# Kernel optimization log

Measured on AMD Instinct MI355X. Metric: run time of the kernel, lower is better.

## Reference

```python
import jax, jax.numpy as jnp
import numpy as np

N_S, N_G, D, K = 30000, 3000, 128, 16
SIGMA = 2.5
BOX = 60.0  # Angstrom box for random coordinates


def setup_inputs() -> dict:
    key = jax.random.key(0)
    ks = jax.random.split(key, 10)
    s = 1.0 / np.sqrt(D)
    return {
        'xs': jax.random.normal(ks[0], (N_S, D), jnp.float32),
        'xg': jax.random.normal(ks[1], (N_G, D), jnp.float32),
        'pos_s': jax.random.uniform(ks[2], (N_S, 3), jnp.float32) * BOX,
        'pos_g': jax.random.uniform(ks[3], (N_G, 3), jnp.float32) * BOX,
        'W_s_pre': jax.random.normal(ks[4], (D, D), jnp.float32) * s,
        'W_g_pre': jax.random.normal(ks[5], (D, D), jnp.float32) * s,
        'W_gs': jax.random.normal(ks[6], (D, D), jnp.float32) * s,
        'W_sg': jax.random.normal(ks[7], (D, D), jnp.float32) * s,
        'W_s_post': jax.random.normal(ks[8], (2 * D, D), jnp.float32) * s,
        'W_g_post': jax.random.normal(ks[9], (2 * D, D), jnp.float32) * s,
        'k': K,
    }


def reference(xs, xg, pos_s, pos_g, W_s_pre, W_g_pre, W_gs, W_sg, W_s_post, W_g_post, k):
    n_s, d = xs.shape
    # ---- compute_bipartite_graphs: knn of each graph node over surface nodes ----
    # squared pairwise distances via gemm form: (N_G, N_S)
    d2 = ((pos_g ** 2).sum(-1)[:, None] + (pos_s ** 2).sum(-1)[None, :]
          - 2.0 * pos_g @ pos_s.T)
    neg_d2, idx = jax.lax.top_k(-d2, k)          # idx: (N_G, K) surface neighbors
    w = jnp.exp(neg_d2 / (2.0 * SIGMA ** 2))     # RBF edge weight exp(-d^2/(2*sigma^2))
    # ---- pre blocks ----
    hs = xs @ W_s_pre                             # (N_S, D)
    hg = xg @ W_g_pre                             # (N_G, D)
    # ---- bp_gs block: graph -> surface weighted edge-conv (scatter-add) ----
    msg_gs = (hg @ W_gs)[:, None, :] * w[:, :, None]          # (N_G, K, D)
    xs_out = jnp.zeros((n_s, d), hs.dtype).at[idx.reshape(-1)].add(
        msg_gs.reshape(-1, d))
    # ---- bp_sg block: surface -> graph weighted edge-conv (gather-sum) ----
    xg_out = ((hs @ W_sg)[idx] * w[:, :, None]).sum(axis=1)   # (N_G, D)
    # ---- post blocks: combine pre features with message output ----
    xs_new = jax.nn.relu(jnp.concatenate([hs, xs_out], axis=-1) @ W_s_post)
    xg_new = jax.nn.relu(jnp.concatenate([hg, xg_out], axis=-1) @ W_g_post)
    return xs_new, xg_new
```

## Files before the change

### kernel.cpp

```cpp
#include <hip/hip_runtime.h>
#include <stdint.h>

#define N_S 30000
#define N_G 3000
#define DD  128
#define KK  16
#define NE  (N_G * KK)
#define NC  16
#define CELLS (NC * NC * NC)
#define CH  3.75f
#define CAP 32

#define FILL_BLOCKS 118
#define PACK_BLOCKS 384
#define KNN_BLOCKS  750
#define NBS 469
#define NBG 47
#define NTILE (NBS + NBG)

using v8s = __attribute__((ext_vector_type(8))) short;
using v4f = __attribute__((ext_vector_type(4))) float;

__device__ __forceinline__ float bf2f(unsigned short u) {
    union { unsigned int i; float f; } v; v.i = ((unsigned int)u) << 16; return v.f;
}
__device__ __forceinline__ unsigned short f2bf(float f) {
    union { float f; unsigned int i; } v; v.f = f;
    unsigned int x = v.i;
    return (unsigned short)((x + 0x7fffu + ((x >> 16) & 1u)) >> 16);
}
__device__ __forceinline__ float ldIn(const void* p, int i, int bf) {
    return bf ? bf2f(((const unsigned short*)p)[i]) : ((const float*)p)[i];
}
__device__ __forceinline__ void stOut(void* p, int i, float v, int bf) {
    if (bf) ((unsigned short*)p)[i] = f2bf(v);
    else    ((float*)p)[i] = v;
}
__device__ __forceinline__ int cellOf(float x) {
    int c = (int)(x * (1.0f / CH));
    if (c < 0) c = 0; if (c > NC - 1) c = NC - 1;
    return c;
}

__device__ __forceinline__ int detectFlag(const void* pos_g) {
    const unsigned int* w = (const unsigned int*)pos_g;
    int votes = 0;
#pragma unroll
    for (int i = 0; i < 16; ++i) {
        const unsigned int b = (w[i] >> 8) & 0xFFu;
        votes += (b >= 0x3Eu && b <= 0x42u) ? 1 : 0;
    }
    return votes >= 8;
}

__device__ void knn_wave(int g, int bf, const void* pos_g,
                         const int* __restrict__ ccnt,
                         const float4* __restrict__ scell,
                         const float4* __restrict__ ovf, int novf,
                         int* __restrict__ idx_out, float* __restrict__ w_out)
{
    const int t = threadIdx.x & 63;

    const float gxf = ldIn(pos_g, 3 * g + 0, bf);
    const float gyf = ldIn(pos_g, 3 * g + 1, bf);
    const float gzf = ldIn(pos_g, 3 * g + 2, bf);
    const double gx = (double)gxf, gy = (double)gyf, gz = (double)gzf;
    const int cx = cellOf(gxf), cy = cellOf(gyf), cz = cellOf(gzf);

    double bk[KK]; int bi[KK];
#pragma unroll
    for (int j = 0; j < KK; ++j) { bk[j] = 1e300; bi[j] = 0x7fffffff; }

    for (int i = t; i < novf; i += 64) {
        const float4 cd = ovf[i];
        const double ddx = gx - (double)cd.x, ddy = gy - (double)cd.y, ddz = gz - (double)cd.z;
        const double d2 = ddx * ddx + ddy * ddy + ddz * ddz;
        const int sidx = __float_as_int(cd.w);
        if (d2 > bk[KK - 1] || (d2 == bk[KK - 1] && sidx > bi[KK - 1])) continue;
        double ck = d2; int ci2 = sidx;
#pragma unroll
        for (int j = 0; j < KK; ++j) {
            const bool less = (ck < bk[j]) || (ck == bk[j] && ci2 < bi[j]);
            const double nk = less ? ck : bk[j]; const int ni = less ? ci2 : bi[j];
            const double ok = less ? bk[j] : ck; const int oi = less ? bi[j] : ci2;
            bk[j] = nk; bi[j] = ni; ck = ok; ci2 = oi;
        }
    }

    bool done = false;
    for (int R = 1; R <= NC && !done; ++R) {
        const int S = 2 * R + 1;
        const int Scells = S * S * S;
        for (int cb = 0; cb < Scells; cb += 64) {
            const int ci = cb + t;
            int cnt = 0, base = 0;
            if (ci < Scells) {
                const int dz = ci % S - R;
                const int dy = (ci / S) % S - R;
                const int dx = ci / (S * S) - R;
                int ax = dx < 0 ? -dx : dx, ay = dy < 0 ? -dy : dy, az = dz < 0 ? -dz : dz;
                int cheb = ax > ay ? ax : ay; if (az > cheb) cheb = az;
                const bool want = (R == 1) ? true : (cheb == R);
                const int X = cx + dx, Y = cy + dy, Z = cz + dz;
                if (want && X >= 0 && X < NC && Y >= 0 && Y < NC && Z >= 0 && Z < NC) {
                    const int cid = (X * NC + Y) * NC + Z;
                    int c = ccnt[cid]; if (c > CAP) c = CAP;
                    cnt = c; base = cid * CAP;
                }
            }
            for (int i = 0; i < cnt; ++i) {
                const float4 cd = scell[base + i];
                const double ddx = gx - (double)cd.x;
                const double ddy = gy - (double)cd.y;
                const double ddz = gz - (double)cd.z;
                const double d2 = ddx * ddx + ddy * ddy + ddz * ddz;
                const int sidx = __float_as_int(cd.w);
                if (d2 > bk[KK - 1]) continue;
                if (d2 == bk[KK - 1] && sidx > bi[KK - 1]) continue;
                double ck = d2; int ci2 = sidx;
#pragma unroll
                for (int j = 0; j < KK; ++j) {
                    const bool less = (ck < bk[j]) || (ck == bk[j] && ci2 < bi[j]);
                    const double nk = less ? ck : bk[j]; const int ni = less ? ci2 : bi[j];
                    const double ok = less ? bk[j] : ck; const int oi = less ? bi[j] : ci2;
                    bk[j] = nk; bi[j] = ni; ck = ok; ci2 = oi;
                }
            }
        }
        double m = 1e300;
        if (cx - R > 0)      { double d = gx - (double)(cx - R) * 3.75; if (d < m) m = d; }
        if (cx + R < NC - 1) { double d = (double)(cx + R + 1) * 3.75 - gx; if (d < m) m = d; }
        if (cy - R > 0)      { double d = gy - (double)(cy - R) * 3.75; if (d < m) m = d; }
        if (cy + R < NC - 1) { double d = (double)(cy + R + 1) * 3.75 - gy; if (d < m) m = d; }
        if (cz - R > 0)      { double d = gz - (double)(cz - R) * 3.75; if (d < m) m = d; }
        if (cz + R < NC - 1) { double d = (double)(cz + R + 1) * 3.75 - gz; if (d < m) m = d; }
        if (m < 0.0) m = 0.0;
        const double m2 = m * m * (1.0 - 1e-12);
        int cntlt = 0;
#pragma unroll
        for (int j = 0; j < KK; ++j) cntlt += (bk[j] < m2) ? 1 : 0;
        for (int d = 1; d < 64; d <<= 1) cntlt += __shfl_xor(cntlt, d);
        if (cntlt >= KK) done = true;
    }

    for (int p = 0; p < KK; ++p) {
        double key = bk[0]; int sid = bi[0];
        for (int d = 1; d < 64; d <<= 1) {
            const double ok = __shfl_xor(key, d);
            const int    os = __shfl_xor(sid, d);
            if (ok < key || (ok == key && os < sid)) { key = ok; sid = os; }
        }
        if (t == 0) {
            idx_out[g * KK + p] = sid;
            w_out[g * KK + p] = expf((float)(-key) * (1.0f / 12.5f));
        }
        const bool win = (bk[0] == key) && (bi[0] == sid);
        if (win) {
#pragma unroll
            for (int j = 0; j < KK - 1; ++j) { bk[j] = bk[j + 1]; bi[j] = bi[j + 1]; }
            bk[KK - 1] = 1e300; bi[KK - 1] = 0x7fffffff;
        }
    }
}

__device__ __forceinline__ v8s loadA_bf16(const unsigned short* p) {
    return *(const v8s*)p;
}
__device__ __forceinline__ v8s loadA_f32v(const float* f) {
    const float4 a = *(const float4*)f;
    const float4 b = *(const float4*)(f + 4);
    v8s r;
    r[0] = (short)f2bf(a.x); r[1] = (short)f2bf(a.y);
    r[2] = (short)f2bf(a.z); r[3] = (short)f2bf(a.w);
    r[4] = (short)f2bf(b.x); r[5] = (short)f2bf(b.y);
    r[6] = (short)f2bf(b.z); r[7] = (short)f2bf(b.w);
    return r;
}
__device__ __forceinline__ v8s loadA_raw(const void* A, size_t off, int bf) {
    if (bf) return loadA_bf16((const unsigned short*)A + off);
    return loadA_f32v((const float*)A + off);
}

__device__ void pre_tile(int task, int bf, const void* xs, const void* xg,
                         const unsigned short* __restrict__ wpk_ps,
                         const unsigned short* __restrict__ wpk_pg,
                         unsigned short* __restrict__ hsb,
                         unsigned short* __restrict__ hgb,
                         float* __restrict__ xs_agg)
{
    const void* A; const unsigned short* wpk; unsigned short* outp; int M, m0;
    const bool is_s = (task < NBS);
    if (is_s) { A = xs; wpk = wpk_ps; outp = hsb; M = N_S; m0 = task * 64; }
    else      { A = xg; wpk = wpk_pg; outp = hgb; M = N_G; m0 = (task - NBS) * 64; }

    const int wave = threadIdx.x >> 6, lane = threadIdx.x & 63;
    const int q = lane >> 4, lm = lane & 15;
    const int mb = m0 + wave * 16;
    const int mrow = mb + lm;
    const bool valid = (mrow < M);

    v4f acc[8];
#pragma unroll
    for (int t = 0; t < 8; ++t) acc[t] = {0.f, 0.f, 0.f, 0.f};
    for (int ks = 0; ks < 4; ++ks) {
        v8s a = {0,0,0,0,0,0,0,0};
        if (valid) a = loadA_raw(A, (size_t)mrow * 128 + ks * 32 + q * 8, bf);
        const unsigned short* wb = wpk + (size_t)(ks * 4 + q) * 128 * 8;
#pragma unroll
        for (int t = 0; t < 8; ++t) {
            const v8s bfr = *(const v8s*)(wb + (t * 16 + lm) * 8);
            acc[t] = __builtin_amdgcn_mfma_f32_16x16x32_bf16(a, bfr, acc[t], 0, 0, 0);
        }
    }
#pragma unroll
    for (int t = 0; t < 8; ++t)
#pragma unroll
        for (int r = 0; r < 4; ++r) {
            const int row = mb + q * 4 + r;
            if (row < M) outp[(size_t)row * 128 + t * 16 + lm] = f2bf(acc[t][r]);
        }
    if (is_s) {
        for (int i = threadIdx.x; i < 64 * 128; i += 256) {
            const int r = m0 + (i >> 7);
            if (r < N_S) xs_agg[(size_t)r * 128 + (i & 127)] = 0.f;
        }
    }
}

__device__ void post_tile(int task, int bf,
                          const unsigned short* __restrict__ hsb,
                          const float* __restrict__ xs_agg,
                          const unsigned short* __restrict__ hgb,
                          const unsigned short* __restrict__ aggg,
                          const unsigned short* __restrict__ wpk_cs,
                          const unsigned short* __restrict__ wpk_cg,
                          void* out)
{
    const unsigned short* A1; const void* A2; int a2f32; const unsigned short* wpk;
    int M, m0, ooff;
    if (task < NBS) { A1 = hsb; A2 = xs_agg; a2f32 = 1; wpk = wpk_cs; M = N_S; m0 = task * 64; ooff = 0; }
    else { A1 = hgb; A2 = aggg; a2f32 = 0; wpk = wpk_cg; M = N_G; m0 = (task - NBS) * 64; ooff = N_S * DD; }

    const int wave = threadIdx.x >> 6, lane = threadIdx.x & 63;
    const int q = lane >> 4, lm = lane & 15;
    const int mb = m0 + wave * 16;
    const int mrow = mb + lm;
    const bool valid = (mrow < M);

    v4f acc[8];
#pragma unroll
    for (int t = 0; t < 8; ++t) acc[t] = {0.f, 0.f, 0.f, 0.f};
    for (int ks = 0; ks < 8; ++ks) {
        const int kk = ks * 32 + q * 8;
        v8s a = {0,0,0,0,0,0,0,0};
        if (valid) {
            if (kk < 128)      a = loadA_bf16(A1 + (size_t)mrow * 128 + kk);
            else if (a2f32)    a = loadA_f32v((const float*)A2 + (size_t)mrow * 128 + (kk - 128));
            else               a = loadA_bf16((const unsigned short*)A2 + (size_t)mrow * 128 + (kk - 128));
        }
        const unsigned short* wb = wpk + (size_t)(ks * 4 + q) * 128 * 8;
#pragma unroll
        for (int t = 0; t < 8; ++t) {
            const v8s bfr = *(const v8s*)(wb + (t * 16 + lm) * 8);
            acc[t] = __builtin_amdgcn_mfma_f32_16x16x32_bf16(a, bfr, acc[t], 0, 0, 0);
        }
    }
#pragma unroll
    for (int t = 0; t < 8; ++t)
#pragma unroll
        for (int r = 0; r < 4; ++r) {
            const int row = mb + q * 4 + r;
            if (row < M) {
                float v = acc[t][r];
                if (v < 0.f) v = 0.f;
                stOut(out, ooff + row * DD + t * 16 + lm, v, bf);
            }
        }
}

__global__ __launch_bounds__(256) void fill_pack_kernel(
    const void* pos_s, const void* pos_g,
    const void* Wsp, const void* Wgp, const void* Wgs, const void* Wsg,
    const void* Wspost, const void* Wgpost,
    int* __restrict__ ccnt, float4* __restrict__ scell,
    float4* __restrict__ ovf, int* __restrict__ novf,
    unsigned short* __restrict__ wpk_ps, unsigned short* __restrict__ wpk_pg,
    unsigned short* __restrict__ wpk_cs, unsigned short* __restrict__ wpk_cg)
{
    const int bf = detectFlag(pos_g);
    const int bid = blockIdx.x, tid = threadIdx.x;
    if (bid < FILL_BLOCKS) {
        const int p = bid * 256 + tid;
        if (p < N_S) {
            const float x = ldIn(pos_s, 3 * p + 0, bf);
            const float y = ldIn(pos_s, 3 * p + 1, bf);
            const float z = ldIn(pos_s, 3 * p + 2, bf);
            const int cid = (cellOf(x) * NC + cellOf(y)) * NC + cellOf(z);
            const int slot = atomicAdd(&ccnt[cid], 1);
            const float4 pt = make_float4(x, y, z, __int_as_float(p));
            if (slot < CAP) scell[cid * CAP + slot] = pt;
            else            ovf[atomicAdd(novf, 1)] = pt;
        }
        return;
    }
    __shared__ float rows[256];
    const int rt = bid - FILL_BLOCKS;
    const int half = tid >> 7, j = tid & 127;
    const int task = rt * 2 + half;
    float v; unsigned short* dst; int k;
    if (task < 128) { k = task; v = ldIn(Wsp, k * DD + j, bf); dst = wpk_ps; }
    else if (task < 256) { k = task - 128; v = ldIn(Wgp, k * DD + j, bf); dst = wpk_pg; }
    else {
        const int which_g = (task >= 512);
        const int r = which_g ? (task - 512) : (task - 256);
        const void* W1 = which_g ? Wsg : Wgs;
        const void* Wp = which_g ? Wgpost : Wspost;
        dst = which_g ? wpk_cg : wpk_cs;
        k = r;
        if (r < 128) v = ldIn(Wp, r * DD + j, bf);
        else {
            rows[half * 128 + j] = ldIn(W1, (r - 128) * DD + j, bf);
            __syncthreads();
            float acc = 0.f;
            for (int m = 0; m < DD; ++m)
                acc += rows[half * 128 + m] * ldIn(Wp, (DD + m) * DD + j, bf);
            v = acc;
        }
    }
    const int ks = k >> 5, q = (k >> 3) & 3, i = k & 7;
    dst[((ks * 4 + q) * 128 + j) * 8 + i] = f2bf(v);
}

__global__ __launch_bounds__(256) void knn_pre_kernel(
    const void* xs, const void* xg, const void* pos_g,
    const int* __restrict__ ccnt, const float4* __restrict__ scell,
    const float4* __restrict__ ovf, const int* __restrict__ novf,
    int* __restrict__ idx, float* __restrict__ w,
    const unsigned short* __restrict__ wpk_ps,
    const unsigned short* __restrict__ wpk_pg,
    unsigned short* __restrict__ hsb, unsigned short* __restrict__ hgb,
    float* __restrict__ xs_agg)
{
    const int bf = detectFlag(pos_g);
    const int bid = blockIdx.x;
    if (bid < KNN_BLOCKS) {
        const int node = bid * 4 + (threadIdx.x >> 6);
        knn_wave(node, bf, pos_g, ccnt, scell, ovf, *novf, idx, w);
    } else {
        pre_tile(bid - KNN_BLOCKS, bf, xs, xg, wpk_ps, wpk_pg, hsb, hgb, xs_agg);
    }
}

__global__ __launch_bounds__(128) void scatgath_kernel(
    const void* pos_g,
    const unsigned short* __restrict__ hsb, const unsigned short* __restrict__ hgb,
    const int* __restrict__ idx, const float* __restrict__ w,
    float* __restrict__ xs_agg, unsigned short* __restrict__ aggg)
{
    const int b = blockIdx.x, j = threadIdx.x;
    if (b < N_G) {
        const float m = bf2f(hgb[b * DD + j]);
#pragma unroll
        for (int k = 0; k < KK; ++k)
            atomicAdd(&xs_agg[(size_t)idx[b * KK + k] * DD + j], m * w[b * KK + k]);
    } else {
        const int g = b - N_G;
        float acc = 0.f;
#pragma unroll
        for (int k = 0; k < KK; ++k)
            acc += w[g * KK + k] * bf2f(hsb[(size_t)idx[g * KK + k] * DD + j]);
        aggg[g * DD + j] = f2bf(acc);
    }
}

__global__ __launch_bounds__(256) void mfma_post_kernel(
    const void* pos_g,
    const unsigned short* __restrict__ hsb, const float* __restrict__ xs_agg,
    const unsigned short* __restrict__ hgb, const unsigned short* __restrict__ aggg,
    const unsigned short* __restrict__ wpk_cs, const unsigned short* __restrict__ wpk_cg,
    void* out)
{
    const int bf = detectFlag(pos_g);
    post_tile(blockIdx.x, bf, hsb, xs_agg, hgb, aggg, wpk_cs, wpk_cg, out);
}

extern "C" void kernel_launch(void* const* d_in, const int* in_sizes, int n_in,
                              void* d_out, int out_size, void* d_ws, size_t ws_size,
                              hipStream_t stream)
{
    const void* xs       = d_in[0];
    const void* xg       = d_in[1];
    const void* pos_s    = d_in[2];
    const void* pos_g    = d_in[3];
    const void* W_s_pre  = d_in[4];
    const void* W_g_pre  = d_in[5];
    const void* W_gs     = d_in[6];
    const void* W_sg     = d_in[7];
    const void* W_s_post = d_in[8];
    const void* W_g_post = d_in[9];
    (void)in_sizes; (void)n_in; (void)out_size; (void)ws_size;

    char* ws = (char*)d_ws;
    size_t off_b = 0;
    auto alloc = [&](size_t bytes) -> void* {
        void* p = ws + off_b;
        off_b = (off_b + bytes + 255) & ~((size_t)255);
        return p;
    };
    unsigned short* hsb    = (unsigned short*)alloc((size_t)N_S * DD * 2);
    unsigned short* hgb    = (unsigned short*)alloc((size_t)N_G * DD * 2);
    unsigned short* aggg   = (unsigned short*)alloc((size_t)N_G * DD * 2);
    float*          xs_agg = (float*) alloc((size_t)N_S * DD * 4);
    unsigned short* wpk_ps = (unsigned short*)alloc((size_t)DD * DD * 2);
    unsigned short* wpk_pg = (unsigned short*)alloc((size_t)DD * DD * 2);
    unsigned short* wpk_cs = (unsigned short*)alloc((size_t)2 * DD * DD * 2);
    unsigned short* wpk_cg = (unsigned short*)alloc((size_t)2 * DD * DD * 2);
    int*            idx    = (int*)   alloc((size_t)NE * 4);
    float*          w      = (float*) alloc((size_t)NE * 4);
    int*            ccnt   = (int*)   alloc((size_t)CELLS * 4 + 4);
    int*            novf   = ccnt + CELLS;
    float4*         scell  = (float4*)alloc((size_t)CELLS * CAP * 16);
    float4*         ovf    = (float4*)alloc((size_t)N_S * 16);

    hipMemsetAsync(ccnt, 0, (size_t)CELLS * 4 + 4, stream);

    fill_pack_kernel<<<FILL_BLOCKS + PACK_BLOCKS, 256, 0, stream>>>(
        pos_s, pos_g, W_s_pre, W_g_pre, W_gs, W_sg, W_s_post, W_g_post,
        ccnt, scell, ovf, novf, wpk_ps, wpk_pg, wpk_cs, wpk_cg);

    knn_pre_kernel<<<KNN_BLOCKS + NTILE, 256, 0, stream>>>(
        xs, xg, pos_g, ccnt, scell, ovf, novf, idx, w,
        wpk_ps, wpk_pg, hsb, hgb, xs_agg);

    scatgath_kernel<<<2 * N_G, 128, 0, stream>>>(pos_g, hsb, hgb, idx, w,
                                                 xs_agg, aggg);

    mfma_post_kernel<<<NTILE, 256, 0, stream>>>(pos_g, hsb, xs_agg, hgb, aggg,
                                                wpk_cs, wpk_cg, d_out);
}
```

Baseline: 211.0 us.

## Load-balance KNN cell scan via prefix-sum compaction, one-wave blocks

KNN candidate evaluation is rebalanced: lanes prefix-sum their cell counts and write a shared-memory map, so points from all cells in a shell are spread evenly across the wave instead of each lane looping over its own cell. The kernel moves to 64-thread blocks (one KNN node or one 16-row pre tile per block), and the cell capacity drops from 32 to 16. Extra barriers and shared-memory traffic are added per shell. Lowering the capacity to 16 risks silently truncating dense cells unless the fill path sends excess points to the overflow list.

New measurement: 196.0 us. -7.1%, faster.

```diff
diff --git a/kernel.cpp b/kernel.cpp
--- a/kernel.cpp
+++ b/kernel.cpp
@@ -9,11 +9,14 @@
 #define NC  16
 #define CELLS (NC * NC * NC)
 #define CH  3.75f
-#define CAP 32
+#define CAP 16
 
 #define FILL_BLOCKS 118
 #define PACK_BLOCKS 384
-#define KNN_BLOCKS  750
+#define KNN_BLOCKS  3000
+#define NBS16 1875
+#define NBG16 188
+#define PRE_TILES (NBS16 + NBG16)
 #define NBS 469
 #define NBG 47
 #define NTILE (NBS + NBG)
@@ -53,13 +56,14 @@
     return votes >= 8;
 }
 
-__device__ void knn_wave(int g, int bf, const void* pos_g,
+__device__ void knn_node(int g, int bf, const void* pos_g,
                          const int* __restrict__ ccnt,
                          const float4* __restrict__ scell,
                          const float4* __restrict__ ovf, int novf,
-                         int* __restrict__ idx_out, float* __restrict__ w_out)
-{
-    const int t = threadIdx.x & 63;
+                         int* __restrict__ idx_out, float* __restrict__ w_out,
+                         unsigned short* map16, int* s_base, int* s_pref)
+{
+    const int t = threadIdx.x;
 
     const float gxf = ldIn(pos_g, 3 * g + 0, bf);
     const float gyf = ldIn(pos_g, 3 * g + 1, bf);
@@ -108,8 +112,19 @@
                     cnt = c; base = cid * CAP;
                 }
             }
-            for (int i = 0; i < cnt; ++i) {
-                const float4 cd = scell[base + i];
+            int incl = cnt;
+            for (int d = 1; d < 64; d <<= 1) {
+                int v = __shfl_up(incl, d);
+                if (t >= d) incl += v;
+            }
+            const int total = __shfl(incl, 63);
+            const int pref = incl - cnt;
+            s_base[t] = base; s_pref[t] = pref;
+            for (int i = 0; i < cnt; ++i) map16[pref + i] = (unsigned short)t;
+            __syncthreads();
+            for (int pos = t; pos < total; pos += 64) {
+                const int slot = map16[pos];
+                const float4 cd = scell[s_base[slot] + (pos - s_pref[slot])];
                 const double ddx = gx - (double)cd.x;
                 const double ddy = gy - (double)cd.y;
                 const double ddz = gz - (double)cd.z;
@@ -126,6 +141,7 @@
                     bk[j] = nk; bi[j] = ni; ck = ok; ci2 = oi;
                 }
             }
+            __syncthreads();
         }
         double m = 1e300;
         if (cx - R > 0)      { double d = gx - (double)(cx - R) * 3.75; if (d < m) m = d; }
@@ -181,22 +197,21 @@
     return loadA_f32v((const float*)A + off);
 }
 
-__device__ void pre_tile(int task, int bf, const void* xs, const void* xg,
-                         const unsigned short* __restrict__ wpk_ps,
-                         const unsigned short* __restrict__ wpk_pg,
-                         unsigned short* __restrict__ hsb,
-                         unsigned short* __restrict__ hgb,
-                         float* __restrict__ xs_agg)
+__device__ void pre_tile16(int task, int bf, const void* xs, const void* xg,
+                           const unsigned short* __restrict__ wpk_ps,
+                           const unsigned short* __restrict__ wpk_pg,
+                           unsigned short* __restrict__ hsb,
+                           unsigned short* __restrict__ hgb,
+                           float* __restrict__ xs_agg)
 {
     const void* A; const unsigned short* wpk; unsigned short* outp; int M, m0;
-    const bool is_s = (task < NBS);
-    if (is_s) { A = xs; wpk = wpk_ps; outp = hsb; M = N_S; m0 = task * 64; }
-    else      { A = xg; wpk = wpk_pg; outp = hgb; M = N_G; m0 = (task - NBS) * 64; }
-
-    const int wave = threadIdx.x >> 6, lane = threadIdx.x & 63;
+    const bool is_s = (task < NBS16);
+    if (is_s) { A = xs; wpk = wpk_ps; outp = hsb; M = N_S; m0 = task * 16; }
+    else      { A = xg; wpk = wpk_pg; outp = hgb; M = N_G; m0 = (task - NBS16) * 16; }
+
+    const int lane = threadIdx.x;
     const int q = lane >> 4, lm = lane & 15;
-    const int mb = m0 + wave * 16;
-    const int mrow = mb + lm;
+    const int mrow = m0 + lm;
     const bool valid = (mrow < M);
 
     v4f acc[8];
@@ -216,14 +231,13 @@
     for (int t = 0; t < 8; ++t)
 #pragma unroll
         for (int r = 0; r < 4; ++r) {
-            const int row = mb + q * 4 + r;
+            const int row = m0 + q * 4 + r;
             if (row < M) outp[(size_t)row * 128 + t * 16 + lm] = f2bf(acc[t][r]);
         }
     if (is_s) {
-        for (int i = threadIdx.x; i < 64 * 128; i += 256) {
-            const int r = m0 + (i >> 7);
-            if (r < N_S) xs_agg[(size_t)r * 128 + (i & 127)] = 0.f;
-        }
+        float4* dst = (float4*)(xs_agg + (size_t)m0 * 128);
+        const float4 z = make_float4(0.f, 0.f, 0.f, 0.f);
+        for (int i = lane; i < 16 * 32; i += 64) dst[i] = z;
     }
 }
 
@@ -331,7 +345,7 @@
     dst[((ks * 4 + q) * 128 + j) * 8 + i] = f2bf(v);
 }
 
-__global__ __launch_bounds__(256) void knn_pre_kernel(
+__global__ __launch_bounds__(64) void knn_pre_kernel(
     const void* xs, const void* xg, const void* pos_g,
     const int* __restrict__ ccnt, const float4* __restrict__ scell,
     const float4* __restrict__ ovf, const int* __restrict__ novf,
@@ -344,15 +358,17 @@
     const int bf = detectFlag(pos_g);
     const int bid = blockIdx.x;
     if (bid < KNN_BLOCKS) {
-        const int node = bid * 4 + (threadIdx.x >> 6);
-        knn_wave(node, bf, pos_g, ccnt, scell, ovf, *novf, idx, w);
+        __shared__ unsigned short map16[64 * CAP];
+        __shared__ int s_base[64];
+        __shared__ int s_pref[64];
+        knn_node(bid, bf, pos_g, ccnt, scell, ovf, *novf, idx, w,
+                 map16, s_base, s_pref);
     } else {
-        pre_tile(bid - KNN_BLOCKS, bf, xs, xg, wpk_ps, wpk_pg, hsb, hgb, xs_agg);
+        pre_tile16(bid - KNN_BLOCKS, bf, xs, xg, wpk_ps, wpk_pg, hsb, hgb, xs_agg);
     }
 }
 
 __global__ __launch_bounds__(128) void scatgath_kernel(
-    const void* pos_g,
     const unsigned short* __restrict__ hsb, const unsigned short* __restrict__ hgb,
     const int* __restrict__ idx, const float* __restrict__ w,
     float* __restrict__ xs_agg, unsigned short* __restrict__ aggg)
@@ -428,11 +444,11 @@
         pos_s, pos_g, W_s_pre, W_g_pre, W_gs, W_sg, W_s_post, W_g_post,
         ccnt, scell, ovf, novf, wpk_ps, wpk_pg, wpk_cs, wpk_cg);
 
-    knn_pre_kernel<<<KNN_BLOCKS + NTILE, 256, 0, stream>>>(
+    knn_pre_kernel<<<KNN_BLOCKS + PRE_TILES, 64, 0, stream>>>(
         xs, xg, pos_g, ccnt, scell, ovf, novf, idx, w,
         wpk_ps, wpk_pg, hsb, hgb, xs_agg);
 
-    scatgath_kernel<<<2 * N_G, 128, 0, stream>>>(pos_g, hsb, hgb, idx, w,
+    scatgath_kernel<<<2 * N_G, 128, 0, stream>>>(hsb, hgb, idx, w,
                                                  xs_agg, aggg);
 
     mfma_post_kernel<<<NTILE, 256, 0, stream>>>(pos_g, hsb, xs_agg, hgb, aggg,
```
